# Performance work log

Measured on AMD Instinct MI355X. Metric: run time of the kernel, lower is better.

## Reference

```python
import jax, jax.numpy as jnp
import numpy as np

N = 4096          # nodes
D_IN = 1024       # in_features
H = 16            # heads
DH = D_IN // H    # d_head
ALPHA = 0.2       # LeakyReLU negative slope
MASK_VAL = -65500.0


def setup_inputs() -> dict:
    key = jax.random.key(0)
    ks = jax.random.split(key, 7)
    x = jax.random.normal(ks[0], (N, D_IN), dtype=jnp.float32)
    adj = jax.random.randint(ks[1], (N, N), 0, 2).astype(jnp.float32)
    s = 1.0 / np.sqrt(D_IN)
    W_seq = jax.random.normal(ks[2], (D_IN, D_IN), dtype=jnp.float32) * s
    a1 = jax.random.normal(ks[3], (DH,), dtype=jnp.float32) / np.sqrt(DH)
    a2 = jax.random.normal(ks[4], (DH,), dtype=jnp.float32) / np.sqrt(DH)
    W_out = jax.random.normal(ks[5], (D_IN, D_IN), dtype=jnp.float32) * s
    b_out = jax.random.normal(ks[6], (D_IN,), dtype=jnp.float32) * 0.01
    return {"x": x, "adj": adj, "W_seq": W_seq, "a1": a1, "a2": a2,
            "W_out": W_out, "b_out": b_out}


def reference(x, adj, W_seq, a1, a2, W_out, b_out):
    # seq: [N, H, DH]
    seq = (x @ W_seq).reshape(N, H, DH)
    # per-head scalar scores: [H, N]
    score1 = jnp.einsum('nhd,d->hn', seq, a1)
    score2 = jnp.einsum('nhd,d->hn', seq, a2)
    # additive attention scores: [H, N, N]
    scores = score1[:, :, None] + score2[:, None, :]
    scores = jax.nn.leaky_relu(scores, negative_slope=ALPHA)
    scores = scores + (1.0 - adj)[None, :, :] * MASK_VAL
    attn = jax.nn.softmax(scores, axis=-1)          # [H, N, N]
    # dropout p=0 -> identity
    hidden = jnp.einsum('hij,jhd->ihd', attn, seq).reshape(N, D_IN)
    hidden = hidden @ W_out + b_out
    # residual=False, concat=True -> ELU
    return jax.nn.elu(hidden)
```

## Files before the change

### kernel.cpp

```cpp
#include <hip/hip_runtime.h>
#include <hip/hip_bf16.h>
#include <math.h>

#define NN 4096
#define DIN 1024
#define NH 16
#define DH 64

typedef unsigned short u16;
typedef unsigned long long u64;
typedef u16 u16x4 __attribute__((ext_vector_type(4)));
typedef u16 u16x8 __attribute__((ext_vector_type(8)));
typedef unsigned ux2 __attribute__((ext_vector_type(2)));
typedef unsigned ux4 __attribute__((ext_vector_type(4)));
typedef float fx4 __attribute__((ext_vector_type(4)));
typedef __bf16 bf16x8 __attribute__((ext_vector_type(8)));
typedef _Float16 h16x8 __attribute__((ext_vector_type(8)));

__device__ __forceinline__ u16 f2b(float f) {
  unsigned u = __float_as_uint(f);
  u += 0x7fff + ((u >> 16) & 1);
  return (u16)(u >> 16);
}
__device__ __forceinline__ float b2f(u16 h) {
  return __uint_as_float(((unsigned)h) << 16);
}
__device__ __forceinline__ u16 f2h_bits(float f) {
  _Float16 h = (_Float16)f;
  return __builtin_bit_cast(unsigned short, h);
}
__device__ __forceinline__ unsigned pack2h(float f) {
  unsigned hb = (unsigned)f2h_bits(f);
  return hb | (hb << 16);
}
__device__ __forceinline__ unsigned pk_mul(unsigned a, unsigned b) {
  unsigned d;
  asm("v_pk_mul_f16 %0, %1, %2" : "=v"(d) : "v"(a), "v"(b));
  return d;
}
__device__ __forceinline__ unsigned pk_max(unsigned a, unsigned b) {
  unsigned d;
  asm("v_pk_max_f16 %0, %1, %2" : "=v"(d) : "v"(a), "v"(b));
  return d;
}
__device__ __forceinline__ void gload16(const void* g, void* l) {
  __builtin_amdgcn_global_load_lds(
      (const __attribute__((address_space(1))) unsigned*)g,
      (__attribute__((address_space(3))) unsigned*)l, 16, 0, 0);
}

__global__ __launch_bounds__(256) void cast_kernel(const float* __restrict__ in,
                                                   u16* __restrict__ out, int n4) {
  int i = blockIdx.x * 256 + threadIdx.x;
  if (i < n4) {
    fx4 v = reinterpret_cast<const fx4*>(in)[i];
    u16x4 o;
    o[0] = f2b(v[0]); o[1] = f2b(v[1]); o[2] = f2b(v[2]); o[3] = f2b(v[3]);
    reinterpret_cast<u16x4*>(out)[i] = o;
  }
}

__global__ __launch_bounds__(256) void tcast_kernel(const float* __restrict__ in,
                                                    u16* __restrict__ out, int R, int C) {
  __shared__ u16 tile[32][33];
  int bc = blockIdx.x * 32, br = blockIdx.y * 32;
  int tx = threadIdx.x & 31, ty = threadIdx.x >> 5;
  #pragma unroll
  for (int r = ty; r < 32; r += 8)
    tile[r][tx] = f2b(in[(size_t)(br + r) * C + bc + tx]);
  __syncthreads();
  #pragma unroll
  for (int r = ty; r < 32; r += 8)
    out[(size_t)(bc + r) * R + br + tx] = tile[tx][r];
}

__global__ __launch_bounds__(256) void tb16h_kernel(const u16* __restrict__ in,
                                                    u16* __restrict__ out, int R, int C) {
  __shared__ u16 tile[32][33];
  int bc = blockIdx.x * 32, br = blockIdx.y * 32;
  int tx = threadIdx.x & 31, ty = threadIdx.x >> 5;
  #pragma unroll
  for (int r = ty; r < 32; r += 8)
    tile[r][tx] = f2h_bits(b2f(in[(size_t)(br + r) * C + bc + tx]));
  __syncthreads();
  #pragma unroll
  for (int r = ty; r < 32; r += 8)
    out[(size_t)(bc + r) * R + br + tx] = tile[tx][r];
}

template <int EPI>
__global__ __launch_bounds__(256, 2) void gemm_bt(const u16* __restrict__ A,
                                                  const u16* __restrict__ BT,
                                                  void* __restrict__ Cv,
                                                  const float* __restrict__ bias,
                                                  int M, int N, int K) {
  __shared__ __align__(16) u16 As[2][128 * 64];
  __shared__ __align__(16) u16 Bs[2][64 * 64];
  const int tid = threadIdx.x;
  const int i0 = blockIdx.x * 128, n0 = blockIdx.y * 64;
  const int w = tid >> 6, l = tid & 63;
  const int wr = w >> 1, wc = w & 1;
  const int lr = l & 15, lslot = l >> 4;
  const int wu = __builtin_amdgcn_readfirstlane(w);
  const int srow_lo = l >> 3, sg = (l & 7) ^ (srow_lo & 7);
  const u16* gA[4];
  #pragma unroll
  for (int jj = 0; jj < 4; jj++)
    gA[jj] = A + (size_t)(i0 + wu * 32 + jj * 8 + srow_lo) * K + sg * 8;
  const u16* gB[2];
  #pragma unroll
  for (int jb = 0; jb < 2; jb++)
    gB[jb] = BT + (size_t)(n0 + wu * 16 + jb * 8 + srow_lo) * K + sg * 8;

  fx4 acc[4][2] = {};

  #pragma unroll
  for (int jj = 0; jj < 4; jj++)
    gload16(gA[jj], (char*)As[0] + wu * 4096 + jj * 1024);
  #pragma unroll
  for (int jb = 0; jb < 2; jb++)
    gload16(gB[jb], (char*)Bs[0] + wu * 2048 + jb * 1024);
  __syncthreads();

  for (int kt = 0; kt < 16; kt++) {
    const int buf = kt & 1;
    if (kt < 15) {
      #pragma unroll
      for (int jj = 0; jj < 4; jj++)
        gload16(gA[jj] + (kt + 1) * 64, (char*)As[buf ^ 1] + wu * 4096 + jj * 1024);
      #pragma unroll
      for (int jb = 0; jb < 2; jb++)
        gload16(gB[jb] + (kt + 1) * 64, (char*)Bs[buf ^ 1] + wu * 2048 + jb * 1024);
    }
    #pragma unroll
    for (int ks = 0; ks < 2; ks++) {
      bf16x8 af[4], bfr[2];
      #pragma unroll
      for (int mi = 0; mi < 4; mi++) {
        const int r = wr * 64 + mi * 16 + lr;
        const int sl = (ks * 4 + lslot) ^ (r & 7);
        af[mi] = *reinterpret_cast<const bf16x8*>((const char*)As[buf] + r * 128 + sl * 16);
      }
      #pragma unroll
      for (int ni = 0; ni < 2; ni++) {
        const int r = wc * 32 + ni * 16 + lr;
        const int sl = (ks * 4 + lslot) ^ (r & 7);
        bfr[ni] = *reinterpret_cast<const bf16x8*>((const char*)Bs[buf] + r * 128 + sl * 16);
      }
      #pragma unroll
      for (int mi = 0; mi < 4; mi++)
        #pragma unroll
        for (int ni = 0; ni < 2; ni++)
          acc[mi][ni] = __builtin_amdgcn_mfma_f32_16x16x32_bf16(af[mi], bfr[ni], acc[mi][ni], 0, 0, 0);
    }
    __syncthreads();
  }

  const int orow = wr * 64 + lslot * 4;
  const int ocol = wc * 32 + lr;
  if (EPI == 0) {
    u16* Cb = (u16*)Cv;
    #pragma unroll
    for (int mi = 0; mi < 4; mi++)
      #pragma unroll
      for (int r = 0; r < 4; r++)
        #pragma unroll
        for (int ni = 0; ni < 2; ni++)
          Cb[(size_t)(i0 + orow + mi * 16 + r) * N + n0 + ocol + ni * 16] = f2b(acc[mi][ni][r]);
  } else {
    float* Cf = (float*)Cv;
    #pragma unroll
    for (int mi = 0; mi < 4; mi++)
      #pragma unroll
      for (int r = 0; r < 4; r++)
        #pragma unroll
        for (int ni = 0; ni < 2; ni++) {
          int col = n0 + ocol + ni * 16;
          float v = acc[mi][ni][r] + bias[col];
          Cf[(size_t)(i0 + orow + mi * 16 + r) * N + col] = v > 0.f ? v : expm1f(v);
        }
  }
}

__global__ __launch_bounds__(256) void scores_kernel(const u16* __restrict__ seqb,
                                                     const float* __restrict__ a1,
                                                     const float* __restrict__ a2,
                                                     float* __restrict__ s1T,
                                                     float* __restrict__ s2H) {
  int n = blockIdx.x, t = threadIdx.x;
  u16x4 v = reinterpret_cast<const u16x4*>(seqb)[n * 256 + t];
  fx4 w1 = reinterpret_cast<const fx4*>(a1)[t & 15];
  fx4 w2 = reinterpret_cast<const fx4*>(a2)[t & 15];
  float s1 = 0.f, s2 = 0.f;
  #pragma unroll
  for (int e = 0; e < 4; e++) {
    float f = b2f(v[e]);
    s1 += f * w1[e];
    s2 += f * w2[e];
  }
  #pragma unroll
  for (int off = 1; off < 16; off <<= 1) {
    s1 += __shfl_xor(s1, off);
    s2 += __shfl_xor(s2, off);
  }
  if ((t & 15) == 0) {
    int h = t >> 4;
    s1T[n * NH + h] = s1;
    s2H[h * NN + n] = s2;
  }
}

__global__ __launch_bounds__(256) void prep_kernel(const float* __restrict__ s2H,
                                                   float* __restrict__ Dmax,
                                                   unsigned* __restrict__ epH2,
                                                   unsigned* __restrict__ enH2) {
  __shared__ float red[4];
  __shared__ float sDm;
  const int h = blockIdx.x, t = threadIdx.x;
  const fx4* d = reinterpret_cast<const fx4*>(s2H + (size_t)h * NN);
  fx4 v[4];
  float mx = -3e38f;
  #pragma unroll
  for (int q = 0; q < 4; q++) {
    v[q] = d[t * 4 + q];
    #pragma unroll
    for (int z = 0; z < 4; z++) mx = fmaxf(mx, v[q][z]);
  }
  #pragma unroll
  for (int off = 1; off < 64; off <<= 1) mx = fmaxf(mx, __shfl_xor(mx, off));
  if ((t & 63) == 0) red[t >> 6] = mx;
  __syncthreads();
  if (t == 0) {
    float m = fmaxf(fmaxf(red[0], red[1]), fmaxf(red[2], red[3]));
    sDm = m;
    Dmax[h] = m;
  }
  __syncthreads();
  const float Dm = sDm;
  #pragma unroll
  for (int q = 0; q < 8; q++) {
    float d0 = v[q >> 1][(q & 1) * 2];
    float d1 = v[q >> 1][(q & 1) * 2 + 1];
    unsigned ep = (unsigned)f2h_bits(__expf(d0 - Dm)) |
                  ((unsigned)f2h_bits(__expf(d1 - Dm)) << 16);
    unsigned en = (unsigned)f2h_bits(__expf(0.2f * (d0 - Dm))) |
                  ((unsigned)f2h_bits(__expf(0.2f * (d1 - Dm))) << 16);
    epH2[h * 2048 + t * 8 + q] = ep;
    enH2[h * 2048 + t * 8 + q] = en;
  }
}

__global__ __launch_bounds__(256) void maskb_kernel(const float* __restrict__ adj,
                                                    unsigned char* __restrict__ mb) {
  size_t g = (size_t)blockIdx.x * 256 + threadIdx.x;
  const fx4* ap = reinterpret_cast<const fx4*>(adj) + g * 4;
  ux4 o;
  #pragma unroll
  for (int q = 0; q < 4; q++) {
    fx4 a = ap[q];
    unsigned b0 = a[0] > 0.5f ? 0xFFu : 0u;
    unsigned b1 = a[1] > 0.5f ? 0xFFu : 0u;
    unsigned b2 = a[2] > 0.5f ? 0xFFu : 0u;
    unsigned b3 = a[3] > 0.5f ? 0xFFu : 0u;
    o[q] = b0 | (b1 << 8) | (b2 << 16) | (b3 << 24);
  }
  reinterpret_cast<ux4*>(mb)[g] = o;
}

__device__ __forceinline__ h16x8 build_p(unsigned Ai2, unsigned Bi2,
                                         ux4 ep, ux4 en, ux2 mk) {
  unsigned w0 = __builtin_amdgcn_perm(0u, mk[0], 0x01010000u);
  unsigned w1 = __builtin_amdgcn_perm(0u, mk[0], 0x03030202u);
  unsigned w2 = __builtin_amdgcn_perm(0u, mk[1], 0x01010000u);
  unsigned w3 = __builtin_amdgcn_perm(0u, mk[1], 0x03030202u);
  ux4 afw;
  afw[0] = pk_max(pk_mul(Ai2, ep[0]), pk_mul(Bi2, en[0])) & w0;
  afw[1] = pk_max(pk_mul(Ai2, ep[1]), pk_mul(Bi2, en[1])) & w1;
  afw[2] = pk_max(pk_mul(Ai2, ep[2]), pk_mul(Bi2, en[2])) & w2;
  afw[3] = pk_max(pk_mul(Ai2, ep[3]), pk_mul(Bi2, en[3])) & w3;
  return __builtin_bit_cast(h16x8, afw);
}

__global__ __launch_bounds__(512, 4) void pv_kernel(const unsigned char* __restrict__ maskB,
                                                    const u16* __restrict__ seqTh,
                                                    const float* __restrict__ s1T,
                                                    const float* __restrict__ Dmax,
                                                    const unsigned* __restrict__ epH2,
                                                    const unsigned* __restrict__ enH2,
                                                    u16* __restrict__ hiddenb) {
  __shared__ __align__(16) u16 Vs[2][64 * 128];
  __shared__ __align__(16) unsigned epL[2048];
  __shared__ __align__(16) unsigned enL[2048];
  const int h = blockIdx.x >> 5, it = blockIdx.x & 31, i0 = it * 128;
  const int t = threadIdx.x, w = t >> 6, l = t & 63;
  const int lr = l & 15, hi = l >> 4, lk = hi * 8;
  const float Dm = Dmax[h];
  const int arow = i0 + w * 16 + lr;
  const float c = s1T[arow * NH + h];
  float mi = c + Dm;
  mi = mi > 0.f ? mi : 0.2f * mi;
  const unsigned Ai2 = pack2h(__expf(c + Dm - mi));
  const unsigned Bi2 = pack2h(__expf(0.2f * (c + Dm) - mi));
  {
    const ux4* gep = reinterpret_cast<const ux4*>(epH2 + h * 2048);
    const ux4* gen = reinterpret_cast<const ux4*>(enH2 + h * 2048);
    ux4 e0 = gep[t];
    ux4 n0 = gen[t];
    *reinterpret_cast<ux4*>(&epL[t * 4]) = e0;
    *reinterpret_cast<ux4*>(&enL[t * 4]) = n0;
  }
  const int wu = __builtin_amdgcn_readfirstlane(w);
  const u16* gsrc[2];
  #pragma unroll
  for (int i = 0; i < 2; i++) {
    int row = wu * 8 + i * 4 + (l >> 4);
    int g = (l & 15) ^ (row & 7);
    gsrc[i] = seqTh + (size_t)(h * DH + row) * NN + g * 8;
  }
  const unsigned char* gm0 = maskB + (size_t)arow * NN + lk;
  fx4 acc[4] = {};
  fx4 acc1 = {};
  h16x8 ones;
  #pragma unroll
  for (int e = 0; e < 8; e++) ones[e] = (_Float16)1.0f;

  #pragma unroll
  for (int i = 0; i < 2; i++)
    gload16(gsrc[i], (char*)Vs[0] + wu * 2048 + i * 1024);
  ux2 mkc[2][2], mkn[2][2];
  #pragma unroll
  for (int jj = 0; jj < 2; jj++)
    #pragma unroll
    for (int ks = 0; ks < 2; ks++)
      mkc[jj][ks] = *reinterpret_cast<const ux2*>(gm0 + jj * 64 + ks * 32);
  __syncthreads();

  for (int JT = 0; JT < 32; JT++) {
    const int buf = JT & 1;
    if (JT < 31) {
      #pragma unroll
      for (int i = 0; i < 2; i++)
        gload16(gsrc[i] + (JT + 1) * 128, (char*)Vs[buf ^ 1] + wu * 2048 + i * 1024);
      const int jn = (JT + 1) * 128;
      #pragma unroll
      for (int jj = 0; jj < 2; jj++)
        #pragma unroll
        for (int ks = 0; ks < 2; ks++)
          mkn[jj][ks] = *reinterpret_cast<const ux2*>(gm0 + jn + jj * 64 + ks * 32);
    }
    #pragma unroll
    for (int jj = 0; jj < 2; jj++) {
      #pragma unroll
      for (int ks = 0; ks < 2; ks++) {
        const int jp = JT * 64 + jj * 32 + ks * 16 + hi * 4;
        ux4 ep = *reinterpret_cast<const ux4*>(&epL[jp]);
        ux4 en = *reinterpret_cast<const ux4*>(&enL[jp]);
        h16x8 bfr[4];
        #pragma unroll
        for (int ni = 0; ni < 4; ni++) {
          const int row = ni * 16 + lr;
          const int colb = (jj * 128 + ks * 64 + hi * 16) ^ ((lr & 7) << 4);
          bfr[ni] = *reinterpret_cast<const h16x8*>((const char*)Vs[buf] + row * 256 + colb);
        }
        h16x8 A = build_p(Ai2, Bi2, ep, en, mkc[jj][ks]);
        #pragma unroll
        for (int ni = 0; ni < 4; ni++)
          acc[ni] = __builtin_amdgcn_mfma_f32_16x16x32_f16(A, bfr[ni], acc[ni], 0, 0, 0);
        acc1 = __builtin_amdgcn_mfma_f32_16x16x32_f16(A, ones, acc1, 0, 0, 0);
      }
    }
    __syncthreads();
    #pragma unroll
    for (int jj = 0; jj < 2; jj++)
      #pragma unroll
      for (int ks = 0; ks < 2; ks++)
        mkc[jj][ks] = mkn[jj][ks];
  }

  #pragma unroll
  for (int r = 0; r < 4; r++) {
    int row = i0 + w * 16 + hi * 4 + r;
    float inv = 1.0f / acc1[r];
    #pragma unroll
    for (int ni = 0; ni < 4; ni++)
      hiddenb[(size_t)row * DIN + h * DH + ni * 16 + lr] = f2b(acc[ni][r] * inv);
  }
}

extern "C" void kernel_launch(void* const* d_in, const int* in_sizes, int n_in,
                              void* d_out, int out_size, void* d_ws, size_t ws_size,
                              hipStream_t stream) {
  const float* x = (const float*)d_in[0];
  const float* adj = (const float*)d_in[1];
  const float* W_seq = (const float*)d_in[2];
  const float* a1 = (const float*)d_in[3];
  const float* a2 = (const float*)d_in[4];
  const float* W_out = (const float*)d_in[5];
  const float* b_out = (const float*)d_in[6];

  char* ws = (char*)d_ws;
  u16* wsT   = (u16*)(ws);
  u16* woT   = (u16*)(ws + (2u << 20));
  u16* seqb  = (u16*)(ws + (4u << 20));
  u16* seqTh = (u16*)(ws + (12u << 20));
  u16* hid   = (u16*)(ws + (20u << 20));
  float* s1T = (float*)(ws + (28u << 20));
  float* s2H = s1T + NN * NH;
  unsigned* epH2 = (unsigned*)(s2H + NN * NH);
  unsigned* enH2 = epH2 + NH * 2048;
  float* DmaxB = (float*)(enH2 + NH * 2048);
  u16* xb = (u16*)(ws + (29u << 20));
  unsigned char* maskB = (unsigned char*)(ws + (29u << 20));

  cast_kernel<<<4096, 256, 0, stream>>>(x, xb, NN * DIN / 4);
  tcast_kernel<<<dim3(32, 32), 256, 0, stream>>>(W_seq, wsT, DIN, DIN);
  tcast_kernel<<<dim3(32, 32), 256, 0, stream>>>(W_out, woT, DIN, DIN);
  gemm_bt<0><<<dim3(32, 16), 256, 0, stream>>>(xb, wsT, (void*)seqb, nullptr, NN, DIN, DIN);
  scores_kernel<<<4096, 256, 0, stream>>>(seqb, a1, a2, s1T, s2H);
  prep_kernel<<<16, 256, 0, stream>>>(s2H, DmaxB, epH2, enH2);
  tb16h_kernel<<<dim3(32, 128), 256, 0, stream>>>(seqb, seqTh, NN, DIN);
  maskb_kernel<<<4096, 256, 0, stream>>>(adj, maskB);
  pv_kernel<<<512, 512, 0, stream>>>(maskB, seqTh, s1T, DmaxB, epH2, enH2, hid);
  gemm_bt<1><<<dim3(32, 16), 256, 0, stream>>>(hid, woT, d_out, b_out, NN, DIN, DIN);
}
```

Baseline: 153.7 us.

## Split PV kernel over key halves with 256-row tiles and add combine pass

Each pv_kernel block now covers 256 query rows (two 16-row m-tiles per wave) over half of the key range instead of 128 rows over all keys. This reuses every staged V tile across twice as many rows, halving V shared-memory traffic per row while keeping the grid at 512 blocks. Unnormalized fp32 partial outputs and row sums are written to workspace, and a new combine kernel adds the two halves, normalizes and casts to bf16. The cost is 32MB of extra fp32 partial writes and reads, one more launch, and higher register pressure from doubled accumulators.

```diff
diff --git a/kernel.cpp b/kernel.cpp
--- a/kernel.cpp
+++ b/kernel.cpp
@@ -287,27 +287,36 @@
                                                     const float* __restrict__ Dmax,
                                                     const unsigned* __restrict__ epH2,
                                                     const unsigned* __restrict__ enH2,
-                                                    u16* __restrict__ hiddenb) {
+                                                    float* __restrict__ part,
+                                                    float* __restrict__ lpart) {
   __shared__ __align__(16) u16 Vs[2][64 * 128];
-  __shared__ __align__(16) unsigned epL[2048];
-  __shared__ __align__(16) unsigned enL[2048];
-  const int h = blockIdx.x >> 5, it = blockIdx.x & 31, i0 = it * 128;
+  __shared__ __align__(16) unsigned epL[1024];
+  __shared__ __align__(16) unsigned enL[1024];
+  const int h = blockIdx.x >> 5, rem = blockIdx.x & 31;
+  const int jh = rem >> 4, it = rem & 15, i0 = it * 256;
+  const int jbase = jh * 2048;
   const int t = threadIdx.x, w = t >> 6, l = t & 63;
   const int lr = l & 15, hi = l >> 4, lk = hi * 8;
   const float Dm = Dmax[h];
-  const int arow = i0 + w * 16 + lr;
-  const float c = s1T[arow * NH + h];
-  float mi = c + Dm;
-  mi = mi > 0.f ? mi : 0.2f * mi;
-  const unsigned Ai2 = pack2h(__expf(c + Dm - mi));
-  const unsigned Bi2 = pack2h(__expf(0.2f * (c + Dm) - mi));
+  unsigned Ai2[2], Bi2[2];
+  int arow[2];
+  #pragma unroll
+  for (int m = 0; m < 2; m++) {
+    int row = i0 + w * 32 + m * 16 + lr;
+    arow[m] = row;
+    float c = s1T[row * NH + h];
+    float mi = c + Dm;
+    mi = mi > 0.f ? mi : 0.2f * mi;
+    Ai2[m] = pack2h(__expf(c + Dm - mi));
+    Bi2[m] = pack2h(__expf(0.2f * (c + Dm) - mi));
+  }
   {
-    const ux4* gep = reinterpret_cast<const ux4*>(epH2 + h * 2048);
-    const ux4* gen = reinterpret_cast<const ux4*>(enH2 + h * 2048);
-    ux4 e0 = gep[t];
-    ux4 n0 = gen[t];
-    *reinterpret_cast<ux4*>(&epL[t * 4]) = e0;
-    *reinterpret_cast<ux4*>(&enL[t * 4]) = n0;
+    if (t < 256)
+      reinterpret_cast<ux4*>(epL)[t] =
+          reinterpret_cast<const ux4*>(epH2 + h * 2048 + jh * 1024)[t];
+    else
+      reinterpret_cast<ux4*>(enL)[t - 256] =
+          reinterpret_cast<const ux4*>(enH2 + h * 2048 + jh * 1024)[t - 256];
   }
   const int wu = __builtin_amdgcn_readfirstlane(w);
   const u16* gsrc[2];
@@ -315,11 +324,12 @@
   for (int i = 0; i < 2; i++) {
     int row = wu * 8 + i * 4 + (l >> 4);
     int g = (l & 15) ^ (row & 7);
-    gsrc[i] = seqTh + (size_t)(h * DH + row) * NN + g * 8;
-  }
-  const unsigned char* gm0 = maskB + (size_t)arow * NN + lk;
-  fx4 acc[4] = {};
-  fx4 acc1 = {};
+    gsrc[i] = seqTh + (size_t)(h * DH + row) * NN + jbase + g * 8;
+  }
+  const unsigned char* gm0 = maskB + (size_t)arow[0] * NN + jbase + lk;
+  const unsigned char* gm1 = maskB + (size_t)arow[1] * NN + jbase + lk;
+  fx4 acc[2][4] = {};
+  fx4 acc1[2] = {};
   h16x8 ones;
   #pragma unroll
   for (int e = 0; e < 8; e++) ones[e] = (_Float16)1.0f;
@@ -327,17 +337,19 @@
   #pragma unroll
   for (int i = 0; i < 2; i++)
     gload16(gsrc[i], (char*)Vs[0] + wu * 2048 + i * 1024);
-  ux2 mkc[2][2], mkn[2][2];
+  ux2 mkc[2][2][2], mkn[2][2][2];
   #pragma unroll
   for (int jj = 0; jj < 2; jj++)
     #pragma unroll
-    for (int ks = 0; ks < 2; ks++)
-      mkc[jj][ks] = *reinterpret_cast<const ux2*>(gm0 + jj * 64 + ks * 32);
-  __syncthreads();
-
-  for (int JT = 0; JT < 32; JT++) {
+    for (int ks = 0; ks < 2; ks++) {
+      mkc[0][jj][ks] = *reinterpret_cast<const ux2*>(gm0 + jj * 64 + ks * 32);
+      mkc[1][jj][ks] = *reinterpret_cast<const ux2*>(gm1 + jj * 64 + ks * 32);
+    }
+  __syncthreads();
+
+  for (int JT = 0; JT < 16; JT++) {
     const int buf = JT & 1;
-    if (JT < 31) {
+    if (JT < 15) {
       #pragma unroll
       for (int i = 0; i < 2; i++)
         gload16(gsrc[i] + (JT + 1) * 128, (char*)Vs[buf ^ 1] + wu * 2048 + i * 1024);
@@ -345,8 +357,10 @@
       #pragma unroll
       for (int jj = 0; jj < 2; jj++)
         #pragma unroll
-        for (int ks = 0; ks < 2; ks++)
-          mkn[jj][ks] = *reinterpret_cast<const ux2*>(gm0 + jn + jj * 64 + ks * 32);
+        for (int ks = 0; ks < 2; ks++) {
+          mkn[0][jj][ks] = *reinterpret_cast<const ux2*>(gm0 + jn + jj * 64 + ks * 32);
+          mkn[1][jj][ks] = *reinterpret_cast<const ux2*>(gm1 + jn + jj * 64 + ks * 32);
+        }
     }
     #pragma unroll
     for (int jj = 0; jj < 2; jj++) {
@@ -362,29 +376,53 @@
           const int colb = (jj * 128 + ks * 64 + hi * 16) ^ ((lr & 7) << 4);
           bfr[ni] = *reinterpret_cast<const h16x8*>((const char*)Vs[buf] + row * 256 + colb);
         }
-        h16x8 A = build_p(Ai2, Bi2, ep, en, mkc[jj][ks]);
-        #pragma unroll
-        for (int ni = 0; ni < 4; ni++)
-          acc[ni] = __builtin_amdgcn_mfma_f32_16x16x32_f16(A, bfr[ni], acc[ni], 0, 0, 0);
-        acc1 = __builtin_amdgcn_mfma_f32_16x16x32_f16(A, ones, acc1, 0, 0, 0);
+        #pragma unroll
+        for (int m = 0; m < 2; m++) {
+          h16x8 A = build_p(Ai2[m], Bi2[m], ep, en, mkc[m][jj][ks]);
+          #pragma unroll
+          for (int ni = 0; ni < 4; ni++)
+            acc[m][ni] = __builtin_amdgcn_mfma_f32_16x16x32_f16(A, bfr[ni], acc[m][ni], 0, 0, 0);
+          acc1[m] = __builtin_amdgcn_mfma_f32_16x16x32_f16(A, ones, acc1[m], 0, 0, 0);
+        }
       }
     }
     __syncthreads();
     #pragma unroll
-    for (int jj = 0; jj < 2; jj++)
-      #pragma unroll
-      for (int ks = 0; ks < 2; ks++)
-        mkc[jj][ks] = mkn[jj][ks];
-  }
-
-  #pragma unroll
-  for (int r = 0; r < 4; r++) {
-    int row = i0 + w * 16 + hi * 4 + r;
-    float inv = 1.0f / acc1[r];
-    #pragma unroll
-    for (int ni = 0; ni < 4; ni++)
-      hiddenb[(size_t)row * DIN + h * DH + ni * 16 + lr] = f2b(acc[ni][r] * inv);
-  }
+    for (int m = 0; m < 2; m++)
+      #pragma unroll
+      for (int jj = 0; jj < 2; jj++)
+        #pragma unroll
+        for (int ks = 0; ks < 2; ks++)
+          mkc[m][jj][ks] = mkn[m][jj][ks];
+  }
+
+  float* pb = part + (size_t)jh * NN * DIN;
+  float* lb = lpart + (size_t)jh * NN * NH;
+  #pragma unroll
+  for (int m = 0; m < 2; m++)
+    #pragma unroll
+    for (int r = 0; r < 4; r++) {
+      int row = i0 + w * 32 + m * 16 + hi * 4 + r;
+      if (lr == 0) lb[row * NH + h] = acc1[m][r];
+      #pragma unroll
+      for (int ni = 0; ni < 4; ni++)
+        pb[(size_t)row * DIN + h * DH + ni * 16 + lr] = acc[m][ni][r];
+    }
+}
+
+__global__ __launch_bounds__(256) void combine_kernel(const float* __restrict__ part,
+                                                      const float* __restrict__ lpart,
+                                                      u16* __restrict__ hid) {
+  const int row = blockIdx.x, t = threadIdx.x;
+  const int h = t >> 4;
+  float lsum = lpart[row * NH + h] + lpart[(size_t)NN * NH + row * NH + h];
+  float inv = 1.0f / lsum;
+  fx4 p0 = reinterpret_cast<const fx4*>(part + (size_t)row * DIN)[t];
+  fx4 p1 = reinterpret_cast<const fx4*>(part + (size_t)NN * DIN + (size_t)row * DIN)[t];
+  u16x4 o;
+  #pragma unroll
+  for (int e = 0; e < 4; e++) o[e] = f2b((p0[e] + p1[e]) * inv);
+  reinterpret_cast<u16x4*>(hid + (size_t)row * DIN)[t] = o;
 }
 
 extern "C" void kernel_launch(void* const* d_in, const int* in_sizes, int n_in,
@@ -411,6 +449,8 @@
   float* DmaxB = (float*)(enH2 + NH * 2048);
   u16* xb = (u16*)(ws + (29u << 20));
   unsigned char* maskB = (unsigned char*)(ws + (29u << 20));
+  float* part  = (float*)(ws + (46u << 20));
+  float* lpart = (float*)(ws + (78u << 20));
 
   cast_kernel<<<4096, 256, 0, stream>>>(x, xb, NN * DIN / 4);
   tcast_kernel<<<dim3(32, 32), 256, 0, stream>>>(W_seq, wsT, DIN, DIN);
@@ -420,6 +460,7 @@
   prep_kernel<<<16, 256, 0, stream>>>(s2H, DmaxB, epH2, enH2);
   tb16h_kernel<<<dim3(32, 128), 256, 0, stream>>>(seqb, seqTh, NN, DIN);
   maskb_kernel<<<4096, 256, 0, stream>>>(adj, maskB);
-  pv_kernel<<<512, 512, 0, stream>>>(maskB, seqTh, s1T, DmaxB, epH2, enH2, hid);
+  pv_kernel<<<512, 512, 0, stream>>>(maskB, seqTh, s1T, DmaxB, epH2, enH2, part, lpart);
+  combine_kernel<<<4096, 256, 0, stream>>>(part, lpart, hid);
   gemm_bt<1><<<dim3(32, 16), 256, 0, stream>>>(hid, woT, d_out, b_out, NN, DIN, DIN);
 }
```

Result: slower. 165.1 us (+7.5%).

## Fuse score reduction and fp16 transpose into the sequence GEMM epilogue

Applied to the files above, without the earlier changes.

Replaces the bf16 seq GEMM, the separate per-node score kernel and the bf16-to-fp16 transpose kernel with one GEMM whose epilogue computes per-head score partials (accumulated with atomics into zeroed buffers) and writes the transposed fp16 seq directly through shared memory. This removes two launches and the write and reread of the full seq buffer. It adds a memset, atomic adds, and a larger epilogue in the GEMM. A sched_barrier is also inserted in the pv_kernel prefetch.

```diff
diff --git a/kernel.cpp b/kernel.cpp
--- a/kernel.cpp
+++ b/kernel.cpp
@@ -74,24 +74,127 @@
     out[(size_t)(bc + r) * R + br + tx] = tile[tx][r];
 }
 
-__global__ __launch_bounds__(256) void tb16h_kernel(const u16* __restrict__ in,
-                                                    u16* __restrict__ out, int R, int C) {
-  __shared__ u16 tile[32][33];
-  int bc = blockIdx.x * 32, br = blockIdx.y * 32;
-  int tx = threadIdx.x & 31, ty = threadIdx.x >> 5;
-  #pragma unroll
-  for (int r = ty; r < 32; r += 8)
-    tile[r][tx] = f2h_bits(b2f(in[(size_t)(br + r) * C + bc + tx]));
-  __syncthreads();
-  #pragma unroll
-  for (int r = ty; r < 32; r += 8)
-    out[(size_t)(bc + r) * R + br + tx] = tile[tx][r];
-}
-
-template <int EPI>
+__global__ __launch_bounds__(256, 2) void gemm_seq(const u16* __restrict__ A,
+                                                   const u16* __restrict__ BT,
+                                                   const float* __restrict__ a1,
+                                                   const float* __restrict__ a2,
+                                                   u16* __restrict__ seqTh,
+                                                   float* __restrict__ s1T,
+                                                   float* __restrict__ s2H,
+                                                   int K) {
+  __shared__ __align__(16) u16 As[2][128 * 64];
+  __shared__ __align__(16) u16 Bs[2][64 * 64];
+  const int tid = threadIdx.x;
+  const int i0 = blockIdx.x * 128, n0 = blockIdx.y * 64, h = blockIdx.y;
+  const int w = tid >> 6, l = tid & 63;
+  const int wr = w >> 1, wc = w & 1;
+  const int lr = l & 15, lslot = l >> 4;
+  const int wu = __builtin_amdgcn_readfirstlane(w);
+  const int srow_lo = l >> 3, sg = (l & 7) ^ (srow_lo & 7);
+  const u16* gA[4];
+  #pragma unroll
+  for (int jj = 0; jj < 4; jj++)
+    gA[jj] = A + (size_t)(i0 + wu * 32 + jj * 8 + srow_lo) * K + sg * 8;
+  const u16* gB[2];
+  #pragma unroll
+  for (int jb = 0; jb < 2; jb++)
+    gB[jb] = BT + (size_t)(n0 + wu * 16 + jb * 8 + srow_lo) * K + sg * 8;
+
+  fx4 acc[4][2] = {};
+
+  #pragma unroll
+  for (int jj = 0; jj < 4; jj++)
+    gload16(gA[jj], (char*)As[0] + wu * 4096 + jj * 1024);
+  #pragma unroll
+  for (int jb = 0; jb < 2; jb++)
+    gload16(gB[jb], (char*)Bs[0] + wu * 2048 + jb * 1024);
+  __syncthreads();
+
+  for (int kt = 0; kt < 16; kt++) {
+    const int buf = kt & 1;
+    if (kt < 15) {
+      #pragma unroll
+      for (int jj = 0; jj < 4; jj++)
+        gload16(gA[jj] + (kt + 1) * 64, (char*)As[buf ^ 1] + wu * 4096 + jj * 1024);
+      #pragma unroll
+      for (int jb = 0; jb < 2; jb++)
+        gload16(gB[jb] + (kt + 1) * 64, (char*)Bs[buf ^ 1] + wu * 2048 + jb * 1024);
+    }
+    #pragma unroll
+    for (int ks = 0; ks < 2; ks++) {
+      bf16x8 af[4], bfr[2];
+      #pragma unroll
+      for (int mi = 0; mi < 4; mi++) {
+        const int r = wr * 64 + mi * 16 + lr;
+        const int sl = (ks * 4 + lslot) ^ (r & 7);
+        af[mi] = *reinterpret_cast<const bf16x8*>((const char*)As[buf] + r * 128 + sl * 16);
+      }
+      #pragma unroll
+      for (int ni = 0; ni < 2; ni++) {
+        const int r = wc * 32 + ni * 16 + lr;
+        const int sl = (ks * 4 + lslot) ^ (r & 7);
+        bfr[ni] = *reinterpret_cast<const bf16x8*>((const char*)Bs[buf] + r * 128 + sl * 16);
+      }
+      #pragma unroll
+      for (int mi = 0; mi < 4; mi++)
+        #pragma unroll
+        for (int ni = 0; ni < 2; ni++)
+          acc[mi][ni] = __builtin_amdgcn_mfma_f32_16x16x32_bf16(af[mi], bfr[ni], acc[mi][ni], 0, 0, 0);
+    }
+    __syncthreads();
+  }
+
+  float a1v[2], a2v[2];
+  #pragma unroll
+  for (int ni = 0; ni < 2; ni++) {
+    int dl = wc * 32 + ni * 16 + lr;
+    a1v[ni] = a1[dl];
+    a2v[ni] = a2[dl];
+  }
+  #pragma unroll
+  for (int mi = 0; mi < 4; mi++)
+    #pragma unroll
+    for (int r = 0; r < 4; r++) {
+      float s1 = acc[mi][0][r] * a1v[0] + acc[mi][1][r] * a1v[1];
+      float s2 = acc[mi][0][r] * a2v[0] + acc[mi][1][r] * a2v[1];
+      #pragma unroll
+      for (int off = 1; off < 16; off <<= 1) {
+        s1 += __shfl_xor(s1, off);
+        s2 += __shfl_xor(s2, off);
+      }
+      if (lr == 0) {
+        int row = i0 + wr * 64 + mi * 16 + lslot * 4 + r;
+        atomicAdd(&s1T[row * NH + h], s1);
+        atomicAdd(&s2H[(size_t)h * NN + row], s2);
+      }
+    }
+
+  u16* tp = (u16*)As;
+  #pragma unroll
+  for (int mi = 0; mi < 4; mi++)
+    #pragma unroll
+    for (int ni = 0; ni < 2; ni++)
+      #pragma unroll
+      for (int rp = 0; rp < 2; rp++) {
+        unsigned pw = (unsigned)f2h_bits(acc[mi][ni][2 * rp]) |
+                      ((unsigned)f2h_bits(acc[mi][ni][2 * rp + 1]) << 16);
+        int d = wc * 32 + ni * 16 + lr;
+        int i = wr * 64 + mi * 16 + lslot * 4 + 2 * rp;
+        *reinterpret_cast<unsigned*>(&tp[d * 132 + i]) = pw;
+      }
+  __syncthreads();
+  const int dd = tid >> 2, ic = (tid & 3) * 32;
+  u16* go = seqTh + (size_t)(h * DH + dd) * NN + i0 + ic;
+  #pragma unroll
+  for (int q = 0; q < 8; q++) {
+    u16x4 v = *reinterpret_cast<const u16x4*>(&tp[dd * 132 + ic + q * 4]);
+    *reinterpret_cast<u16x4*>(go + q * 4) = v;
+  }
+}
+
 __global__ __launch_bounds__(256, 2) void gemm_bt(const u16* __restrict__ A,
                                                   const u16* __restrict__ BT,
-                                                  void* __restrict__ Cv,
+                                                  float* __restrict__ Cf,
                                                   const float* __restrict__ bias,
                                                   int M, int N, int K) {
   __shared__ __align__(16) u16 As[2][128 * 64];
@@ -158,56 +261,16 @@
 
   const int orow = wr * 64 + lslot * 4;
   const int ocol = wc * 32 + lr;
-  if (EPI == 0) {
-    u16* Cb = (u16*)Cv;
-    #pragma unroll
-    for (int mi = 0; mi < 4; mi++)
-      #pragma unroll
-      for (int r = 0; r < 4; r++)
-        #pragma unroll
-        for (int ni = 0; ni < 2; ni++)
-          Cb[(size_t)(i0 + orow + mi * 16 + r) * N + n0 + ocol + ni * 16] = f2b(acc[mi][ni][r]);
-  } else {
-    float* Cf = (float*)Cv;
-    #pragma unroll
-    for (int mi = 0; mi < 4; mi++)
-      #pragma unroll
-      for (int r = 0; r < 4; r++)
-        #pragma unroll
-        for (int ni = 0; ni < 2; ni++) {
-          int col = n0 + ocol + ni * 16;
-          float v = acc[mi][ni][r] + bias[col];
-          Cf[(size_t)(i0 + orow + mi * 16 + r) * N + col] = v > 0.f ? v : expm1f(v);
-        }
-  }
-}
-
-__global__ __launch_bounds__(256) void scores_kernel(const u16* __restrict__ seqb,
-                                                     const float* __restrict__ a1,
-                                                     const float* __restrict__ a2,
-                                                     float* __restrict__ s1T,
-                                                     float* __restrict__ s2H) {
-  int n = blockIdx.x, t = threadIdx.x;
-  u16x4 v = reinterpret_cast<const u16x4*>(seqb)[n * 256 + t];
-  fx4 w1 = reinterpret_cast<const fx4*>(a1)[t & 15];
-  fx4 w2 = reinterpret_cast<const fx4*>(a2)[t & 15];
-  float s1 = 0.f, s2 = 0.f;
-  #pragma unroll
-  for (int e = 0; e < 4; e++) {
-    float f = b2f(v[e]);
-    s1 += f * w1[e];
-    s2 += f * w2[e];
-  }
-  #pragma unroll
-  for (int off = 1; off < 16; off <<= 1) {
-    s1 += __shfl_xor(s1, off);
-    s2 += __shfl_xor(s2, off);
-  }
-  if ((t & 15) == 0) {
-    int h = t >> 4;
-    s1T[n * NH + h] = s1;
-    s2H[h * NN + n] = s2;
-  }
+  #pragma unroll
+  for (int mi = 0; mi < 4; mi++)
+    #pragma unroll
+    for (int r = 0; r < 4; r++)
+      #pragma unroll
+      for (int ni = 0; ni < 2; ni++) {
+        int col = n0 + ocol + ni * 16;
+        float v = acc[mi][ni][r] + bias[col];
+        Cf[(size_t)(i0 + orow + mi * 16 + r) * N + col] = v > 0.f ? v : expm1f(v);
+      }
 }
 
 __global__ __launch_bounds__(256) void prep_kernel(const float* __restrict__ s2H,
@@ -347,6 +410,7 @@
         #pragma unroll
         for (int ks = 0; ks < 2; ks++)
           mkn[jj][ks] = *reinterpret_cast<const ux2*>(gm0 + jn + jj * 64 + ks * 32);
+      __builtin_amdgcn_sched_barrier(0);
     }
     #pragma unroll
     for (int jj = 0; jj < 2; jj++) {
@@ -401,7 +465,6 @@
   char* ws = (char*)d_ws;
   u16* wsT   = (u16*)(ws);
   u16* woT   = (u16*)(ws + (2u << 20));
-  u16* seqb  = (u16*)(ws + (4u << 20));
   u16* seqTh = (u16*)(ws + (12u << 20));
   u16* hid   = (u16*)(ws + (20u << 20));
   float* s1T = (float*)(ws + (28u << 20));
@@ -415,11 +478,10 @@
   cast_kernel<<<4096, 256, 0, stream>>>(x, xb, NN * DIN / 4);
   tcast_kernel<<<dim3(32, 32), 256, 0, stream>>>(W_seq, wsT, DIN, DIN);
   tcast_kernel<<<dim3(32, 32), 256, 0, stream>>>(W_out, woT, DIN, DIN);
-  gemm_bt<0><<<dim3(32, 16), 256, 0, stream>>>(xb, wsT, (void*)seqb, nullptr, NN, DIN, DIN);
-  scores_kernel<<<4096, 256, 0, stream>>>(seqb, a1, a2, s1T, s2H);
+  hipMemsetAsync(s1T, 0, 2u * NN * NH * sizeof(float), stream);
+  gemm_seq<<<dim3(32, 16), 256, 0, stream>>>(xb, wsT, a1, a2, seqTh, s1T, s2H, DIN);
   prep_kernel<<<16, 256, 0, stream>>>(s2H, DmaxB, epH2, enH2);
-  tb16h_kernel<<<dim3(32, 128), 256, 0, stream>>>(seqb, seqTh, NN, DIN);
   maskb_kernel<<<4096, 256, 0, stream>>>(adj, maskB);
   pv_kernel<<<512, 512, 0, stream>>>(maskB, seqTh, s1T, DmaxB, epH2, enH2, hid);
-  gemm_bt<1><<<dim3(32, 16), 256, 0, stream>>>(hid, woT, d_out, b_out, NN, DIN, DIN);
-}
+  gemm_bt<<<dim3(32, 16), 256, 0, stream>>>(hid, woT, (float*)d_out, b_out, NN, DIN, DIN);
+}
```

Result: no change. 154.4 us (+0.4%).
